# Optimization experiments

Measured on AMD Instinct MI355X. Metric: run time of the kernel, lower is better.

Reference implementation:

```python
import jax, jax.numpy as jnp
import numpy as np

D = 1024  # d = D_in // 3
GAMMA = 5.0
EPS_NORM = 1e-5
EPS_W = 1e-8


def batch_affine_norm(x, g, b):
    # normalize over batch+time dims, per-feature affine
    mean = x.mean(axis=(0, 1))
    var = x.var(axis=(0, 1))
    return (x - mean) / jnp.sqrt(var + EPS_NORM) * g + b


def block(xi, w, b, a, g, beta):
    # xi: (B,T,d) -> (B,T,d,3)
    # PositiveLinearHK(1->3): softplus-positive weight + bias, per channel
    h = xi[..., None] * jax.nn.softplus(w) + b          # (B,T,d,3)
    # SingleStiefelProjector(3): orthogonalize learned 3x3 via QR, apply
    Q, _ = jnp.linalg.qr(a)                             # (d,3,3)
    h = jnp.einsum('btdi,dij->btdj', h, Q)
    return batch_affine_norm(h, g, beta)


def setup_inputs() -> dict:
    key = jax.random.key(0)
    ks = jax.random.split(key, 20)
    B, T = 4, 2048
    inp = {'x': jax.random.normal(ks[0], (B, T, 3 * D), dtype=jnp.float32)}
    i = 1
    for p in ('q', 'k', 'v'):
        inp['w' + p] = jax.random.normal(ks[i], (D, 3), dtype=jnp.float32) * 0.5; i += 1
        inp['b' + p] = jnp.zeros((D, 3), dtype=jnp.float32)
        inp['a' + p] = jax.random.normal(ks[i], (D, 3, 3), dtype=jnp.float32); i += 1
        inp['g' + p] = jnp.ones((D, 3), dtype=jnp.float32)
        inp['beta' + p] = jnp.zeros((D, 3), dtype=jnp.float32)
    inp['g_out'] = jnp.ones((D,), dtype=jnp.float32)
    inp['b_out'] = jnp.zeros((D,), dtype=jnp.float32)
    return inp


def reference(x, wq, bq, aq, gq, betaq, wk, bk, ak, gk, betak, wv, bv, av, gv, betav, g_out, b_out):
    d = D
    Qp = block(x[..., :d], wq, bq, aq, gq, betaq)        # (B,T,d,3)
    Kp = block(x[..., d:2 * d], wk, bk, ak, gk, betak)
    Vp = block(x[..., 2 * d:], wv, bv, av, gv, betav)
    scores = jax.nn.sigmoid(GAMMA * (Qp * Kp))
    weights = scores / (scores.sum(axis=-1, keepdims=True) + EPS_W)
    out = (weights * Vp).sum(axis=-1)                    # (B,T,d)
    return batch_affine_norm(out, g_out, b_out)
```

## Files before the change

kernel.cpp:

```cpp
#include <hip/hip_runtime.h>
#include <hip/hip_fp16.h>
#include <math.h>

namespace {

constexpr int DD = 1024;
constexpr int NC = 3072;
constexpr int NG = 768;
constexpr int DG = 256;
constexpr int NROWS = 8192;
constexpr float GAMMA = 5.0f;
constexpr float EPS_NORM = 1e-5f;
constexpr float EPS_W = 1e-8f;
constexpr float ZCLAMP = 15.0f;

typedef float nfloat4 __attribute__((ext_vector_type(4)));

struct Params {
  const float *x;
  const float *wq, *aq, *gq, *betaq;
  const float *wk, *ak, *gk, *betak;
  const float *wv, *av, *gv, *betav;
  const float *g_out, *b_out;
  float *out;
  float *colsum, *colsq;
  float *osum, *osq;
  unsigned short *o_arr;
};

__device__ __forceinline__ void acc4(float4& s, float4& q, float4 v) {
  s.x += v.x; s.y += v.y; s.z += v.z; s.w += v.w;
  q.x += v.x * v.x; q.y += v.y * v.y; q.z += v.z * v.z; q.w += v.w * v.w;
}

__device__ __forceinline__ void qr_coef_reg(const Params& P, int c, float mean,
                                            float var, float* Aout, float* Bout) {
  int p = c >> 10;
  int d = c & (DD - 1);
  const float* w    = (p == 0) ? P.wq    : (p == 1) ? P.wk    : P.wv;
  const float* a    = (p == 0) ? P.aq    : (p == 1) ? P.ak    : P.av;
  const float* g    = (p == 0) ? P.gq    : (p == 1) ? P.gk    : P.gv;
  const float* beta = (p == 0) ? P.betaq : (p == 1) ? P.betak : P.betav;
  float gam = (p == 0) ? GAMMA : 1.0f;

  float A[3][3];
  #pragma unroll
  for (int i = 0; i < 3; ++i)
    #pragma unroll
    for (int j = 0; j < 3; ++j) A[i][j] = a[(d * 3 + i) * 3 + j];

  float v1y = 0.f, v1z = 0.f, v2z = 0.f, t1 = 0.f, t2 = 0.f;
  {
    float alpha = A[0][0];
    float xn2 = A[1][0] * A[1][0] + A[2][0] * A[2][0];
    if (xn2 > 0.f) {
      float beta_ = -copysignf(sqrtf(alpha * alpha + xn2), alpha);
      t1 = (beta_ - alpha) / beta_;
      float inv = 1.0f / (alpha - beta_);
      v1y = A[1][0] * inv; v1z = A[2][0] * inv;
      #pragma unroll
      for (int j = 1; j < 3; ++j) {
        float dot = A[0][j] + A[1][j] * v1y + A[2][j] * v1z;
        float f = t1 * dot;
        A[0][j] -= f; A[1][j] -= f * v1y; A[2][j] -= f * v1z;
      }
    }
  }
  {
    float alpha = A[1][1], x2 = A[2][1];
    if (x2 != 0.f) {
      float beta_ = -copysignf(sqrtf(alpha * alpha + x2 * x2), alpha);
      t2 = (beta_ - alpha) / beta_;
      v2z = x2 / (alpha - beta_);
    }
  }
  float v1[3] = {1.f, v1y, v1z};
  float v2[3] = {0.f, 1.f, v2z};
  float v12 = v1y + v1z * v2z;
  float sp0 = log1pf(expf(w[d * 3 + 0]));
  float sp1 = log1pf(expf(w[d * 3 + 1]));
  float sp2 = log1pf(expf(w[d * 3 + 2]));
  #pragma unroll
  for (int j = 0; j < 3; ++j) {
    float Q0 = ((0 == j) ? 1.f : 0.f) - t1 * v1[0] * v1[j] - t2 * v2[0] * v2[j]
               + t1 * t2 * v12 * v1[0] * v2[j];
    float Q1 = ((1 == j) ? 1.f : 0.f) - t1 * v1[1] * v1[j] - t2 * v2[1] * v2[j]
               + t1 * t2 * v12 * v1[1] * v2[j];
    float Q2 = ((2 == j) ? 1.f : 0.f) - t1 * v1[2] * v1[j] - t2 * v2[2] * v2[j]
               + t1 * t2 * v12 * v1[2] * v2[j];
    float W = sp0 * Q0 + sp1 * Q1 + sp2 * Q2;
    float s = W * g[d * 3 + j] / sqrtf(W * W * var + EPS_NORM);
    Aout[j] = gam * s;
    Bout[j] = gam * (beta[d * 3 + j] - mean * s);
  }
}

struct CoefReg {
  float4 Aq[3], Bq[3], Ak[3], Bk[3], Av[3], Bv[3];
};

__device__ __forceinline__ float4 contract4(float4 xq, float4 xk, float4 xv,
                                            const CoefReg& C) {
  float4 ov;
  #pragma unroll
  for (int kk = 0; kk < 4; ++kk) {
    float xqv = ((const float*)&xq)[kk];
    float xkv = ((const float*)&xk)[kk];
    float xvv = ((const float*)&xv)[kk];
    float Q[3], K[3], V[3];
    #pragma unroll
    for (int j = 0; j < 3; ++j) {
      Q[j] = fmaf(xqv, ((const float*)&C.Aq[j])[kk], ((const float*)&C.Bq[j])[kk]);
      K[j] = fmaf(xkv, ((const float*)&C.Ak[j])[kk], ((const float*)&C.Bk[j])[kk]);
      V[j] = fmaf(xvv, ((const float*)&C.Av[j])[kk], ((const float*)&C.Bv[j])[kk]);
    }
    float e0 = __expf(fminf(Q[0] * K[0], ZCLAMP));
    float e1 = __expf(fminf(Q[1] * K[1], ZCLAMP));
    float e2 = __expf(fminf(Q[2] * K[2], ZCLAMP));
    float a0 = 1.f + e0, a1 = 1.f + e1, a2 = 1.f + e2;
    float a01 = a0 * a1, a12 = a1 * a2, a02 = a0 * a2;
    float w0 = e0 * a12, w1 = e1 * a02, w2 = e2 * a01;
    float num = w0 * V[0] + w1 * V[1] + w2 * V[2];
    float den = w0 + w1 + w2 + EPS_W * (a01 * a2);
    ((float*)&ov)[kk] = num / den;
  }
  return ov;
}

__global__ __launch_bounds__(256, 4) void k1_col_stats(Params P) {
  __shared__ float4 lds_s[4][64];
  __shared__ float4 lds_q[4][64];
  const int t = threadIdx.x;
  const int lane = t & 63;
  const int slice = t >> 6;
  const int cg = blockIdx.x * 64 + lane;
  const int r0 = blockIdx.y * 128 + slice * 32;
  const float4* x4 = (const float4*)P.x;
  float4 s = {0,0,0,0}, q = {0,0,0,0};
  #pragma unroll 8
  for (int r = 0; r < 32; ++r) {
    acc4(s, q, x4[(size_t)(r0 + r) * NG + cg]);
  }
  lds_s[slice][lane] = s;
  lds_q[slice][lane] = q;
  __syncthreads();
  float ssum = 0.f, ssq = 0.f;
  #pragma unroll
  for (int i = 0; i < 4; ++i) {
    ssum += ((const float*)&lds_s[i][t >> 2])[t & 3];
    ssq  += ((const float*)&lds_q[i][t >> 2])[t & 3];
  }
  atomicAdd(&P.colsum[blockIdx.x * 256 + t], ssum);
  atomicAdd(&P.colsq[blockIdx.x * 256 + t], ssq);
}

__global__ __launch_bounds__(256, 3) void k2_main(Params P) {
  __shared__ float lds_A[3][256][3];
  __shared__ float lds_B[3][256][3];
  __shared__ float4 lds_s[4][64];
  __shared__ float4 lds_q[4][64];
  const int t = threadIdx.x;
  const int lane = t & 63;
  const int slice = t >> 6;
  const int tg = blockIdx.x * 64 + lane;
  const int r0 = blockIdx.y * 32 + slice * 8;

  {
    const int dcol = blockIdx.x * 256 + t;
    float s = 0.f, q = 0.f, mean, var;
    #pragma unroll
    for (int p = 0; p < 3; ++p) {
      int c = p * DD + dcol;
      s = P.colsum[c];
      q = P.colsq[c];
      mean = s / NROWS;
      var = q / NROWS - mean * mean;
      if (var < 0.f) var = 0.f;
      float Ac[3], Bc[3];
      qr_coef_reg(P, c, mean, var, Ac, Bc);
      #pragma unroll
      for (int j = 0; j < 3; ++j) {
        lds_A[p][t][j] = Ac[j];
        lds_B[p][t][j] = Bc[j];
      }
    }
  }
  __syncthreads();

  CoefReg C;
  {
    const int gl = (lane << 2);
    #pragma unroll
    for (int j = 0; j < 3; ++j) {
      #pragma unroll
      for (int kk = 0; kk < 4; ++kk) {
        ((float*)&C.Aq[j])[kk] = lds_A[0][gl + kk][j];
        ((float*)&C.Bq[j])[kk] = lds_B[0][gl + kk][j];
        ((float*)&C.Ak[j])[kk] = lds_A[1][gl + kk][j];
        ((float*)&C.Bk[j])[kk] = lds_B[1][gl + kk][j];
        ((float*)&C.Av[j])[kk] = lds_A[2][gl + kk][j];
        ((float*)&C.Bv[j])[kk] = lds_B[2][gl + kk][j];
      }
    }
  }

  const float4* x4 = (const float4*)P.x;
  ushort4* o4 = (ushort4*)P.o_arr;
  float4 s = {0,0,0,0}, q = {0,0,0,0};
  #pragma unroll
  for (int r = 0; r < 8; ++r) {
    size_t base = (size_t)(r0 + r) * NG;
    float4 xq = x4[base + tg];
    float4 xk = x4[base + 256 + tg];
    float4 xv = x4[base + 512 + tg];
    float4 ov = contract4(xq, xk, xv, C);
    ushort4 oh;
    oh.x = __half_as_ushort(__float2half(ov.x));
    oh.y = __half_as_ushort(__float2half(ov.y));
    oh.z = __half_as_ushort(__float2half(ov.z));
    oh.w = __half_as_ushort(__float2half(ov.w));
    o4[(size_t)(r0 + r) * DG + tg] = oh;
    acc4(s, q, ov);
  }
  lds_s[slice][lane] = s;
  lds_q[slice][lane] = q;
  __syncthreads();
  float ssum = 0.f, ssq = 0.f;
  #pragma unroll
  for (int i = 0; i < 4; ++i) {
    ssum += ((const float*)&lds_s[i][t >> 2])[t & 3];
    ssq  += ((const float*)&lds_q[i][t >> 2])[t & 3];
  }
  atomicAdd(&P.osum[blockIdx.x * 256 + t], ssum);
  atomicAdd(&P.osq[blockIdx.x * 256 + t], ssq);
}

__global__ __launch_bounds__(256, 8) void k3_final(Params P) {
  const int t = threadIdx.x;
  float4 s4 = ((const float4*)P.osum)[t];
  float4 q4 = ((const float4*)P.osq)[t];
  float4 g4 = ((const float4*)P.g_out)[t];
  float4 b4 = ((const float4*)P.b_out)[t];
  float4 m, sc;
  #pragma unroll
  for (int kk = 0; kk < 4; ++kk) {
    float mean = ((const float*)&s4)[kk] / NROWS;
    float var = ((const float*)&q4)[kk] / NROWS - mean * mean;
    if (var < 0.f) var = 0.f;
    ((float*)&m)[kk] = mean;
    ((float*)&sc)[kk] = ((const float*)&g4)[kk] / sqrtf(var + EPS_NORM);
  }
  const int r0 = blockIdx.x * 4;
  const ushort4* o4 = (const ushort4*)P.o_arr;
  float4* out4 = (float4*)P.out;
  #pragma unroll
  for (int rr = 0; rr < 4; ++rr) {
    size_t idx = (size_t)(r0 + rr) * DG + t;
    ushort4 oh = o4[idx];
    nfloat4 y;
    y.x = (__half2float(__ushort_as_half(oh.x)) - m.x) * sc.x + b4.x;
    y.y = (__half2float(__ushort_as_half(oh.y)) - m.y) * sc.y + b4.y;
    y.z = (__half2float(__ushort_as_half(oh.z)) - m.z) * sc.z + b4.z;
    y.w = (__half2float(__ushort_as_half(oh.w)) - m.w) * sc.w + b4.w;
    __builtin_nontemporal_store(y, (nfloat4*)&out4[idx]);
  }
}

}

extern "C" void kernel_launch(void* const* d_in, const int* in_sizes, int n_in,
                              void* d_out, int out_size, void* d_ws, size_t ws_size,
                              hipStream_t stream) {
  Params P;
  P.x     = (const float*)d_in[0];
  P.wq    = (const float*)d_in[1];
  P.aq    = (const float*)d_in[3];
  P.gq    = (const float*)d_in[4];
  P.betaq = (const float*)d_in[5];
  P.wk    = (const float*)d_in[6];
  P.ak    = (const float*)d_in[8];
  P.gk    = (const float*)d_in[9];
  P.betak = (const float*)d_in[10];
  P.wv    = (const float*)d_in[11];
  P.av    = (const float*)d_in[13];
  P.gv    = (const float*)d_in[14];
  P.betav = (const float*)d_in[15];
  P.g_out = (const float*)d_in[16];
  P.b_out = (const float*)d_in[17];
  P.out   = (float*)d_out;

  float* ws = (float*)d_ws;
  P.colsum = ws;  ws += NC;
  P.colsq  = ws;  ws += NC;
  P.osum   = ws;  ws += DD;
  P.osq    = ws;  ws += DD;
  P.o_arr  = (unsigned short*)ws;

  (void)hipMemsetAsync(P.colsum, 0, (2 * NC + 2 * DD) * sizeof(float), stream);
  k1_col_stats<<<dim3(12, 64), dim3(256), 0, stream>>>(P);
  k2_main<<<dim3(4, 256), dim3(256), 0, stream>>>(P);
  k3_final<<<dim3(2048), dim3(256), 0, stream>>>(P);
}
```

Before: 65.11 us.

## Fuse main contraction and output normalization via cooperative grid sync

Adds a cooperative kernel that computes the contraction, keeps each thread's outputs in registers, accumulates the output column statistics, then uses a grid-wide sync to apply the final normalization directly. This removes the fp16 intermediate write and re-read and the separate finalize launch. It also halves rows per block in the column-stats kernel to launch more blocks. It depends on all 1024 blocks being co-resident (4 per CU are needed). If the cooperative launch fails, it falls back to the old three-kernel path.

After: 214.9 us. +230.0%, slower.

```diff
diff --git a/kernel.cpp b/kernel.cpp
--- a/kernel.cpp
+++ b/kernel.cpp
@@ -1,6 +1,9 @@
 #include <hip/hip_runtime.h>
+#include <hip/hip_cooperative_groups.h>
 #include <hip/hip_fp16.h>
 #include <math.h>
+
+namespace cg = cooperative_groups;
 
 namespace {
 
@@ -127,6 +130,48 @@
   return ov;
 }
 
+__device__ __forceinline__ void qr_prologue(const Params& P, int t, int bx,
+                                            float (*lds_A)[256][3],
+                                            float (*lds_B)[256][3]) {
+  const int dcol = bx * 256 + t;
+  #pragma unroll
+  for (int p = 0; p < 3; ++p) {
+    int c = p * DD + dcol;
+    float s = P.colsum[c];
+    float q = P.colsq[c];
+    float mean = s / NROWS;
+    float var = q / NROWS - mean * mean;
+    if (var < 0.f) var = 0.f;
+    float Ac[3], Bc[3];
+    qr_coef_reg(P, c, mean, var, Ac, Bc);
+    #pragma unroll
+    for (int j = 0; j < 3; ++j) {
+      lds_A[p][t][j] = Ac[j];
+      lds_B[p][t][j] = Bc[j];
+    }
+  }
+}
+
+__device__ __forceinline__ CoefReg gather_coefs(int lane,
+                                                const float (*lds_A)[256][3],
+                                                const float (*lds_B)[256][3]) {
+  CoefReg C;
+  const int gl = (lane << 2);
+  #pragma unroll
+  for (int j = 0; j < 3; ++j) {
+    #pragma unroll
+    for (int kk = 0; kk < 4; ++kk) {
+      ((float*)&C.Aq[j])[kk] = lds_A[0][gl + kk][j];
+      ((float*)&C.Bq[j])[kk] = lds_B[0][gl + kk][j];
+      ((float*)&C.Ak[j])[kk] = lds_A[1][gl + kk][j];
+      ((float*)&C.Bk[j])[kk] = lds_B[1][gl + kk][j];
+      ((float*)&C.Av[j])[kk] = lds_A[2][gl + kk][j];
+      ((float*)&C.Bv[j])[kk] = lds_B[2][gl + kk][j];
+    }
+  }
+  return C;
+}
+
 __global__ __launch_bounds__(256, 4) void k1_col_stats(Params P) {
   __shared__ float4 lds_s[4][64];
   __shared__ float4 lds_q[4][64];
@@ -134,11 +179,11 @@
   const int lane = t & 63;
   const int slice = t >> 6;
   const int cg = blockIdx.x * 64 + lane;
-  const int r0 = blockIdx.y * 128 + slice * 32;
+  const int r0 = blockIdx.y * 64 + slice * 16;
   const float4* x4 = (const float4*)P.x;
   float4 s = {0,0,0,0}, q = {0,0,0,0};
   #pragma unroll 8
-  for (int r = 0; r < 32; ++r) {
+  for (int r = 0; r < 16; ++r) {
     acc4(s, q, x4[(size_t)(r0 + r) * NG + cg]);
   }
   lds_s[slice][lane] = s;
@@ -152,6 +197,82 @@
   }
   atomicAdd(&P.colsum[blockIdx.x * 256 + t], ssum);
   atomicAdd(&P.colsq[blockIdx.x * 256 + t], ssq);
+}
+
+__global__ __launch_bounds__(256, 4) void k2_coop(Params P) {
+  cg::grid_group grid = cg::this_grid();
+  __shared__ float lds_A[3][256][3];
+  __shared__ float lds_B[3][256][3];
+  __shared__ float4 lds_s[4][64];
+  __shared__ float4 lds_q[4][64];
+  const int t = threadIdx.x;
+  const int lane = t & 63;
+  const int slice = t >> 6;
+  const int tg = blockIdx.x * 64 + lane;
+  const int r0 = blockIdx.y * 32 + slice * 8;
+
+  qr_prologue(P, t, blockIdx.x, lds_A, lds_B);
+  __syncthreads();
+  CoefReg C = gather_coefs(lane, lds_A, lds_B);
+
+  const float4* x4 = (const float4*)P.x;
+  float4 osave[8];
+  float4 s = {0,0,0,0}, q = {0,0,0,0};
+  #pragma unroll
+  for (int r = 0; r < 8; ++r) {
+    size_t base = (size_t)(r0 + r) * NG;
+    float4 xq = x4[base + tg];
+    float4 xk = x4[base + 256 + tg];
+    float4 xv = x4[base + 512 + tg];
+    float4 ov = contract4(xq, xk, xv, C);
+    osave[r] = ov;
+    acc4(s, q, ov);
+  }
+  lds_s[slice][lane] = s;
+  lds_q[slice][lane] = q;
+  __syncthreads();
+  {
+    float ssum = 0.f, ssq = 0.f;
+    #pragma unroll
+    for (int i = 0; i < 4; ++i) {
+      ssum += ((const float*)&lds_s[i][t >> 2])[t & 3];
+      ssq  += ((const float*)&lds_q[i][t >> 2])[t & 3];
+    }
+    atomicAdd(&P.osum[blockIdx.x * 256 + t], ssum);
+    atomicAdd(&P.osq[blockIdx.x * 256 + t], ssq);
+  }
+
+  grid.sync();
+
+  float4 m, sc;
+  {
+    float4 g4 = ((const float4*)P.g_out)[tg];
+    #pragma unroll
+    for (int kk = 0; kk < 4; ++kk) {
+      int d = tg * 4 + kk;
+      float ssum = __hip_atomic_load(&P.osum[d], __ATOMIC_RELAXED,
+                                     __HIP_MEMORY_SCOPE_AGENT);
+      float ssq  = __hip_atomic_load(&P.osq[d], __ATOMIC_RELAXED,
+                                     __HIP_MEMORY_SCOPE_AGENT);
+      float mean = ssum / NROWS;
+      float var = ssq / NROWS - mean * mean;
+      if (var < 0.f) var = 0.f;
+      ((float*)&m)[kk] = mean;
+      ((float*)&sc)[kk] = ((const float*)&g4)[kk] / sqrtf(var + EPS_NORM);
+    }
+  }
+  float4 b4 = ((const float4*)P.b_out)[tg];
+  float4* out4 = (float4*)P.out;
+  #pragma unroll
+  for (int r = 0; r < 8; ++r) {
+    float4 o = osave[r];
+    nfloat4 y;
+    y.x = (o.x - m.x) * sc.x + b4.x;
+    y.y = (o.y - m.y) * sc.y + b4.y;
+    y.z = (o.z - m.z) * sc.z + b4.z;
+    y.w = (o.w - m.w) * sc.w + b4.w;
+    __builtin_nontemporal_store(y, (nfloat4*)&out4[(size_t)(r0 + r) * DG + tg]);
+  }
 }
 
 __global__ __launch_bounds__(256, 3) void k2_main(Params P) {
@@ -165,44 +286,9 @@
   const int tg = blockIdx.x * 64 + lane;
   const int r0 = blockIdx.y * 32 + slice * 8;
 
-  {
-    const int dcol = blockIdx.x * 256 + t;
-    float s = 0.f, q = 0.f, mean, var;
-    #pragma unroll
-    for (int p = 0; p < 3; ++p) {
-      int c = p * DD + dcol;
-      s = P.colsum[c];
-      q = P.colsq[c];
-      mean = s / NROWS;
-      var = q / NROWS - mean * mean;
-      if (var < 0.f) var = 0.f;
-      float Ac[3], Bc[3];
-      qr_coef_reg(P, c, mean, var, Ac, Bc);
-      #pragma unroll
-      for (int j = 0; j < 3; ++j) {
-        lds_A[p][t][j] = Ac[j];
-        lds_B[p][t][j] = Bc[j];
-      }
-    }
-  }
-  __syncthreads();
-
-  CoefReg C;
-  {
-    const int gl = (lane << 2);
-    #pragma unroll
-    for (int j = 0; j < 3; ++j) {
-      #pragma unroll
-      for (int kk = 0; kk < 4; ++kk) {
-        ((float*)&C.Aq[j])[kk] = lds_A[0][gl + kk][j];
-        ((float*)&C.Bq[j])[kk] = lds_B[0][gl + kk][j];
-        ((float*)&C.Ak[j])[kk] = lds_A[1][gl + kk][j];
-        ((float*)&C.Bk[j])[kk] = lds_B[1][gl + kk][j];
-        ((float*)&C.Av[j])[kk] = lds_A[2][gl + kk][j];
-        ((float*)&C.Bv[j])[kk] = lds_B[2][gl + kk][j];
-      }
-    }
-  }
+  qr_prologue(P, t, blockIdx.x, lds_A, lds_B);
+  __syncthreads();
+  CoefReg C = gather_coefs(lane, lds_A, lds_B);
 
   const float4* x4 = (const float4*)P.x;
   ushort4* o4 = (ushort4*)P.o_arr;
@@ -297,7 +383,15 @@
   P.o_arr  = (unsigned short*)ws;
 
   (void)hipMemsetAsync(P.colsum, 0, (2 * NC + 2 * DD) * sizeof(float), stream);
-  k1_col_stats<<<dim3(12, 64), dim3(256), 0, stream>>>(P);
+  k1_col_stats<<<dim3(12, 128), dim3(256), 0, stream>>>(P);
+
+  void* kargs[] = {(void*)&P};
+  hipError_t err = hipLaunchCooperativeKernel((const void*)k2_coop,
+                                              dim3(4, 256), dim3(256),
+                                              kargs, 0, stream);
+  if (err == hipSuccess) return;
+  (void)hipGetLastError();
+
   k2_main<<<dim3(4, 256), dim3(256), 0, stream>>>(P);
   k3_final<<<dim3(2048), dim3(256), 0, stream>>>(P);
 }
```
